# Kernel tuning notes

Measured on AMD Instinct MI355X. Metric: run time of the kernel, lower is better.

Reference implementation:

```python
import jax, jax.numpy as jnp
import numpy as np

SAMP_RATE = 24000
HARMONIC_NUM = 8
DIM = HARMONIC_NUM + 1
SINE_AMP = 0.1
NOISE_STD = 0.003
VOICED_THRESHOLD = 0.0
B, L = 16, 240000


def setup_inputs() -> dict:
    key = jax.random.key(0)
    k_f0, k_voiced, k_ini, k_noise, k_w = jax.random.split(key, 5)
    f0 = jax.random.uniform(k_f0, (B, L, 1), jnp.float32, 80.0, 400.0)
    voiced = (jax.random.uniform(k_voiced, (B, L, 1)) > 0.2).astype(jnp.float32)
    f0 = f0 * voiced
    # random initial phase per (batch, harmonic); fundamental gets phase 0
    rand_ini = jax.random.uniform(k_ini, (B, DIM), jnp.float32)
    rand_ini = rand_ini.at[:, 0].set(0.0)
    noise = jax.random.normal(k_noise, (B, L, DIM), jnp.float32)
    merge_w = jax.random.normal(k_w, (1, DIM), jnp.float32) / np.sqrt(DIM)
    return {"f0": f0, "rand_ini": rand_ini, "noise": noise, "merge_w": merge_w}


def reference(f0, rand_ini, noise, merge_w):
    # f0_buf: fundamental plus harmonics -> (B, L, DIM)
    harmonics = jnp.arange(1, DIM + 1, dtype=f0.dtype)  # [1, 2, ..., DIM]
    f0_buf = f0 * harmonics  # broadcast (B,L,1)*(DIM,)

    # normalized instantaneous frequency in cycles/sample, with random init phase
    rad_values = jnp.mod(f0_buf / SAMP_RATE, 1.0)
    rad_values = rad_values.at[:, 0, :].add(rand_ini)

    # phase-wrap correction: detect where cumsum%1 wraps, subtract 1 there
    tmp_over_one = jnp.mod(jnp.cumsum(rad_values, axis=1), 1.0)
    wrap = (tmp_over_one[:, 1:, :] - tmp_over_one[:, :-1, :]) < 0
    cumsum_shift = jnp.concatenate(
        [jnp.zeros_like(rad_values[:, :1, :]), -wrap.astype(rad_values.dtype)], axis=1
    )
    phase = jnp.cumsum(rad_values + cumsum_shift, axis=1)
    sine_waves = jnp.sin(phase * (2.0 * jnp.pi)) * SINE_AMP

    # voiced/unvoiced mask and noise injection
    uv = (f0 > VOICED_THRESHOLD).astype(f0.dtype)  # (B, L, 1)
    noise_amp = uv * NOISE_STD + (1.0 - uv) * (SINE_AMP / 3.0)
    sine_waves = sine_waves * uv + noise_amp * noise

    # merge: Linear(DIM, 1, bias=False) + tanh
    out = jnp.tanh(jnp.einsum("bld,od->blo", sine_waves, merge_w))
    return out
```

## Files before the change

kernel.cpp:

```cpp
#include <hip/hip_runtime.h>
#include <math.h>

namespace {
constexpr int kB = 16;
constexpr int kL = 240000;
constexpr int kD = 9;
constexpr float kInvSamp = 1.0f / 24000.0f;
constexpr int kChunk = 2048;
constexpr int kT = 8;
constexpr int kThreads = 256;
constexpr int kNChunks = 118;
constexpr float kSineAmp = 0.1f;
constexpr float kNoiseStd = 0.003f;
constexpr float kNoiseUnv = (float)(0.1 / 3.0);
}

__global__ __launch_bounds__(kThreads) void sine_pass_a(
    const float* __restrict__ f0, double* __restrict__ agg) {
  const int c = blockIdx.x, b = blockIdx.y, tid = threadIdx.x;
  const int l0 = c * kChunk + tid * kT;
  float s = 0.0f;
  if (l0 < kL) {
    const float4* f4 = reinterpret_cast<const float4*>(f0 + (size_t)b * kL + l0);
    const float4 a = f4[0], bb = f4[1];
    s = ((a.x + a.y) + (a.z + a.w)) + ((bb.x + bb.y) + (bb.z + bb.w));
  }
  double v = (double)s * (double)kInvSamp;
#pragma unroll
  for (int ofs = 1; ofs < 64; ofs <<= 1) v += __shfl_xor(v, ofs, 64);
  __shared__ double wt[4];
  const int wid = tid >> 6;
  if ((tid & 63) == 0) wt[wid] = v;
  __syncthreads();
  if (tid == 0) agg[(size_t)b * kNChunks + c] = wt[0] + wt[1] + wt[2] + wt[3];
}

__global__ __launch_bounds__(kThreads) void sine_emit(
    const float* __restrict__ f0, const float* __restrict__ rand_ini,
    const float* __restrict__ noise, const float* __restrict__ w,
    const double* __restrict__ agg, float* __restrict__ out) {
  const int c = blockIdx.x, b = blockIdx.y, tid = threadIdx.x;
  const int lane = tid & 63, wid = tid >> 6;
  const int l0 = c * kChunk + tid * kT;
  const bool active = l0 < kL;

  float rq[kT];
  float tsum = 0.0f;
  if (active) {
    const float4* f4 = reinterpret_cast<const float4*>(f0 + (size_t)b * kL + l0);
    const float4 a = f4[0], bb = f4[1];
    rq[0] = a.x * kInvSamp; rq[1] = a.y * kInvSamp;
    rq[2] = a.z * kInvSamp; rq[3] = a.w * kInvSamp;
    rq[4] = bb.x * kInvSamp; rq[5] = bb.y * kInvSamp;
    rq[6] = bb.z * kInvSamp; rq[7] = bb.w * kInvSamp;
#pragma unroll
    for (int j = 0; j < kT; ++j) tsum += rq[j];
  } else {
#pragma unroll
    for (int j = 0; j < kT; ++j) rq[j] = 0.0f;
  }

  double pv = (tid < c) ? agg[(size_t)b * kNChunks + tid] : 0.0;

  float nz[kT * kD];
  if (active) {
    const float4* n4 =
        reinterpret_cast<const float4*>(noise + ((size_t)b * kL + l0) * kD);
#pragma unroll
    for (int i = 0; i < 18; ++i) {
      const float4 x = n4[i];
      nz[4 * i + 0] = x.x; nz[4 * i + 1] = x.y;
      nz[4 * i + 2] = x.z; nz[4 * i + 3] = x.w;
    }
  }

#pragma unroll
  for (int ofs = 1; ofs < 64; ofs <<= 1) pv += __shfl_xor(pv, ofs, 64);

  double incl = (double)tsum;
#pragma unroll
  for (int ofs = 1; ofs < 64; ofs <<= 1) {
    const double u = __shfl_up(incl, ofs, 64);
    if (lane >= ofs) incl += u;
  }

  __shared__ double rtot[4], wtot[4];
  if (lane == 0) rtot[wid] = pv;
  if (lane == 63) wtot[wid] = incl;
  __syncthreads();

  if (!active) return;

  double base = rtot[0] + rtot[1] + rtot[2] + rtot[3];
#pragma unroll
  for (int k = 0; k < 4; ++k)
    if (k < wid) base += wtot[k];
  const double cbase = base + incl - (double)tsum;

  float basef[kD], wv[kD];
#pragma unroll
  for (int d = 0; d < kD; ++d) {
    const double ph = (double)(d + 1) * cbase + (double)rand_ini[b * kD + d];
    basef[d] = (float)(ph - floor(ph));
    wv[d] = w[d];
  }

  float ob[kT];
  float pref = 0.0f;
#pragma unroll
  for (int j = 0; j < kT; ++j) {
    pref += rq[j];
    const float f = rq[j];
    const float au = (f > 0.0f) ? kSineAmp : 0.0f;
    const float namp = (f > 0.0f) ? kNoiseStd : kNoiseUnv;
    float dots = 0.0f, dotn = 0.0f;
#pragma unroll
    for (int d = 0; d < kD; ++d) {
      const float pf = __builtin_amdgcn_fractf(basef[d] + (float)(d + 1) * pref);
      const float sv = __builtin_amdgcn_sinf(pf);
      dots = fmaf(wv[d], sv, dots);
      dotn = fmaf(wv[d], nz[j * kD + d], dotn);
    }
    const float x = au * dots + namp * dotn;
    const float e = __expf(2.0f * x);
    ob[j] = 1.0f - 2.0f * __builtin_amdgcn_rcpf(e + 1.0f);
  }

  float4* o4 = reinterpret_cast<float4*>(out + (size_t)b * kL + l0);
  o4[0] = make_float4(ob[0], ob[1], ob[2], ob[3]);
  o4[1] = make_float4(ob[4], ob[5], ob[6], ob[7]);
}

extern "C" void kernel_launch(void* const* d_in, const int* in_sizes, int n_in,
                              void* d_out, int out_size, void* d_ws,
                              size_t ws_size, hipStream_t stream) {
  const float* f0 = (const float*)d_in[0];
  const float* rand_ini = (const float*)d_in[1];
  const float* noise = (const float*)d_in[2];
  const float* w = (const float*)d_in[3];
  float* out = (float*)d_out;
  double* agg = (double*)d_ws;

  const dim3 grid(kNChunks, kB), block(kThreads);
  sine_pass_a<<<grid, block, 0, stream>>>(f0, agg);
  sine_emit<<<grid, block, 0, stream>>>(f0, rand_ini, noise, w, agg, out);
}
```

Before: 35.12 us.

## Halve chunk size and stage noise through LDS with coalesced loads

```diff
diff --git a/kernel.cpp b/kernel.cpp
--- a/kernel.cpp
+++ b/kernel.cpp
@@ -6,10 +6,11 @@
 constexpr int kL = 240000;
 constexpr int kD = 9;
 constexpr float kInvSamp = 1.0f / 24000.0f;
-constexpr int kChunk = 2048;
-constexpr int kT = 8;
+constexpr int kChunk = 1024;
+constexpr int kT = 4;
 constexpr int kThreads = 256;
-constexpr int kNChunks = 118;
+constexpr int kNChunks = 235;
+constexpr int kN4Full = kChunk * kD / 4;
 constexpr float kSineAmp = 0.1f;
 constexpr float kNoiseStd = 0.003f;
 constexpr float kNoiseUnv = (float)(0.1 / 3.0);
@@ -21,9 +22,8 @@
   const int l0 = c * kChunk + tid * kT;
   float s = 0.0f;
   if (l0 < kL) {
-    const float4* f4 = reinterpret_cast<const float4*>(f0 + (size_t)b * kL + l0);
-    const float4 a = f4[0], bb = f4[1];
-    s = ((a.x + a.y) + (a.z + a.w)) + ((bb.x + bb.y) + (bb.z + bb.w));
+    const float4 a = *reinterpret_cast<const float4*>(f0 + (size_t)b * kL + l0);
+    s = (a.x + a.y) + (a.z + a.w);
   }
   double v = (double)s * (double)kInvSamp;
 #pragma unroll
@@ -39,6 +39,8 @@
     const float* __restrict__ f0, const float* __restrict__ rand_ini,
     const float* __restrict__ noise, const float* __restrict__ w,
     const double* __restrict__ agg, float* __restrict__ out) {
+  __shared__ float4 nlds[kN4Full];
+  __shared__ double rtot[4], wtot[4];
   const int c = blockIdx.x, b = blockIdx.y, tid = threadIdx.x;
   const int lane = tid & 63, wid = tid >> 6;
   const int l0 = c * kChunk + tid * kT;
@@ -47,14 +49,10 @@
   float rq[kT];
   float tsum = 0.0f;
   if (active) {
-    const float4* f4 = reinterpret_cast<const float4*>(f0 + (size_t)b * kL + l0);
-    const float4 a = f4[0], bb = f4[1];
+    const float4 a = *reinterpret_cast<const float4*>(f0 + (size_t)b * kL + l0);
     rq[0] = a.x * kInvSamp; rq[1] = a.y * kInvSamp;
     rq[2] = a.z * kInvSamp; rq[3] = a.w * kInvSamp;
-    rq[4] = bb.x * kInvSamp; rq[5] = bb.y * kInvSamp;
-    rq[6] = bb.z * kInvSamp; rq[7] = bb.w * kInvSamp;
-#pragma unroll
-    for (int j = 0; j < kT; ++j) tsum += rq[j];
+    tsum = rq[0] + rq[1] + rq[2] + rq[3];
   } else {
 #pragma unroll
     for (int j = 0; j < kT; ++j) rq[j] = 0.0f;
@@ -62,16 +60,15 @@
 
   double pv = (tid < c) ? agg[(size_t)b * kNChunks + tid] : 0.0;
 
-  float nz[kT * kD];
-  if (active) {
-    const float4* n4 =
-        reinterpret_cast<const float4*>(noise + ((size_t)b * kL + l0) * kD);
+  const int n4avail = (c == kNChunks - 1) ? ((kL - c * kChunk) * kD / 4)
+                                          : kN4Full;
+  const float4* n4 = reinterpret_cast<const float4*>(
+      noise + ((size_t)b * kL + (size_t)c * kChunk) * kD);
+  float4 st[9];
 #pragma unroll
-    for (int i = 0; i < 18; ++i) {
-      const float4 x = n4[i];
-      nz[4 * i + 0] = x.x; nz[4 * i + 1] = x.y;
-      nz[4 * i + 2] = x.z; nz[4 * i + 3] = x.w;
-    }
+  for (int k = 0; k < 9; ++k) {
+    const int idx = k * kThreads + tid;
+    if (idx < n4avail) st[k] = n4[idx];
   }
 
 #pragma unroll
@@ -84,9 +81,14 @@
     if (lane >= ofs) incl += u;
   }
 
-  __shared__ double rtot[4], wtot[4];
   if (lane == 0) rtot[wid] = pv;
   if (lane == 63) wtot[wid] = incl;
+
+#pragma unroll
+  for (int k = 0; k < 9; ++k) {
+    const int idx = k * kThreads + tid;
+    if (idx < n4avail) nlds[idx] = st[k];
+  }
   __syncthreads();
 
   if (!active) return;
@@ -103,6 +105,14 @@
     const double ph = (double)(d + 1) * cbase + (double)rand_ini[b * kD + d];
     basef[d] = (float)(ph - floor(ph));
     wv[d] = w[d];
+  }
+
+  float nz[kT * kD];
+#pragma unroll
+  for (int i = 0; i < 9; ++i) {
+    const float4 x = nlds[tid * 9 + i];
+    nz[4 * i + 0] = x.x; nz[4 * i + 1] = x.y;
+    nz[4 * i + 2] = x.z; nz[4 * i + 3] = x.w;
   }
 
   float ob[kT];
@@ -126,9 +136,8 @@
     ob[j] = 1.0f - 2.0f * __builtin_amdgcn_rcpf(e + 1.0f);
   }
 
-  float4* o4 = reinterpret_cast<float4*>(out + (size_t)b * kL + l0);
-  o4[0] = make_float4(ob[0], ob[1], ob[2], ob[3]);
-  o4[1] = make_float4(ob[4], ob[5], ob[6], ob[7]);
+  *reinterpret_cast<float4*>(out + (size_t)b * kL + l0) =
+      make_float4(ob[0], ob[1], ob[2], ob[3]);
 }
 
 extern "C" void kernel_launch(void* const* d_in, const int* in_sizes, int n_in,
```

New measurement: 75.55 us. +115.1%, slower.
